# Optimization experiments

Measured on AMD Instinct MI355X. Metric: run time of the kernel, lower is better.

## Reference

```python
import jax, jax.numpy as jnp
import numpy as np

N, IN_C, HID, H1, E, EP = 4096, 256, 128, 4, 131072, 131072
TH, TL, FF = 4, 2, 512  # transformer heads, layers, ffn dim
D = HID  # transformer d_model


def setup_inputs() -> dict:
    key = jax.random.key(0)
    ks = jax.random.split(key, 32)
    s = 0.05
    inp = {
        'features': jax.random.normal(ks[0], (N, IN_C), jnp.float32),
        'src': jax.random.randint(ks[1], (E,), 0, N),
        'dst': jax.random.randint(ks[2], (E,), 0, N),
        'psrc': jax.random.randint(ks[3], (EP,), 0, N),
        'pdst': jax.random.randint(ks[4], (EP,), 0, N),
        # GAT layer 1: in=256 -> heads=4, out=128
        'W1': jax.random.normal(ks[5], (H1 * HID, IN_C), jnp.float32) * s,
        'al1': jax.random.normal(ks[6], (H1, HID), jnp.float32) * s,
        'ar1': jax.random.normal(ks[7], (H1, HID), jnp.float32) * s,
        'b1': jnp.zeros((H1 * HID,), jnp.float32),
        # GAT layer 2: in=512 -> heads=1, out=128
        'W2': jax.random.normal(ks[8], (HID, H1 * HID), jnp.float32) * s,
        'al2': jax.random.normal(ks[9], (1, HID), jnp.float32) * s,
        'ar2': jax.random.normal(ks[10], (1, HID), jnp.float32) * s,
        'b2': jnp.zeros((HID,), jnp.float32),
        # Transformer encoder (TL layers, torch TransformerEncoderLayer post-norm, relu)
        'tw_qkv': jax.random.normal(ks[11], (TL, 3 * D, D), jnp.float32) * s,
        'tb_qkv': jnp.zeros((TL, 3 * D), jnp.float32),
        'tw_o': jax.random.normal(ks[12], (TL, D, D), jnp.float32) * s,
        'tb_o': jnp.zeros((TL, D), jnp.float32),
        'ln1_g': jnp.ones((TL, D), jnp.float32),
        'ln1_b': jnp.zeros((TL, D), jnp.float32),
        'tw_ff1': jax.random.normal(ks[13], (TL, FF, D), jnp.float32) * s,
        'tb_ff1': jnp.zeros((TL, FF), jnp.float32),
        'tw_ff2': jax.random.normal(ks[14], (TL, D, FF), jnp.float32) * s,
        'tb_ff2': jnp.zeros((TL, D), jnp.float32),
        'ln2_g': jnp.ones((TL, D), jnp.float32),
        'ln2_b': jnp.zeros((TL, D), jnp.float32),
        # decoder MLP
        'fc1_w': jax.random.normal(ks[15], (HID, 2 * HID), jnp.float32) * s,
        'fc1_b': jnp.zeros((HID,), jnp.float32),
        'fc2_w': jax.random.normal(ks[16], (1, HID), jnp.float32) * s,
        'fc2_b': jnp.zeros((1,), jnp.float32),
    }
    return inp


def _leaky(x):
    return jnp.where(x > 0, x, 0.2 * x)


def _gat(x, W, al, ar, b, src, dst, n):
    H, F = al.shape
    h = (x @ W.T).reshape(n, H, F)  # [N,H,F]
    el = jnp.sum(h * al[None], -1)  # [N,H]
    er = jnp.sum(h * ar[None], -1)
    e = _leaky(el[src] + er[dst])  # [E,H]
    m = jax.ops.segment_max(e, dst, num_segments=n)
    ex = jnp.exp(e - m[dst])
    ssum = jax.ops.segment_sum(ex, dst, num_segments=n)
    alpha = ex / ssum[dst]  # edge softmax over incoming edges of dst
    out = jax.ops.segment_sum(h[src] * alpha[:, :, None], dst, num_segments=n)
    return out + b.reshape(1, H, F)


def _ln(x, g, b):
    mu = jnp.mean(x, -1, keepdims=True)
    var = jnp.mean((x - mu) ** 2, -1, keepdims=True)
    return (x - mu) / jnp.sqrt(var + 1e-5) * g + b


def _encoder_layer(h, wqkv, bqkv, wo, bo, g1, b1, wf1, bf1, wf2, bf2, g2, b2):
    n, d = h.shape
    hd = d // TH
    qkv = h @ wqkv.T + bqkv
    q, k, v = jnp.split(qkv, 3, axis=-1)
    q = q.reshape(n, TH, hd)
    k = k.reshape(n, TH, hd)
    v = v.reshape(n, TH, hd)
    scores = jnp.einsum('qhd,khd->hqk', q, k) / jnp.sqrt(jnp.float32(hd))
    attn = jax.nn.softmax(scores, axis=-1)
    o = jnp.einsum('hqk,khd->qhd', attn, v).reshape(n, d) @ wo.T + bo
    h = _ln(h + o, g1, b1)
    ff = jax.nn.relu(h @ wf1.T + bf1) @ wf2.T + bf2
    return _ln(h + ff, g2, b2)


def reference(features, W1, al1, ar1, b1, W2, al2, ar2, b2,
              tw_qkv, tb_qkv, tw_o, tb_o, ln1_g, ln1_b,
              tw_ff1, tb_ff1, tw_ff2, tb_ff2, ln2_g, ln2_b,
              fc1_w, fc1_b, fc2_w, fc2_b, src, dst, psrc, pdst):
    n = features.shape[0]
    h = _gat(features, W1, al1, ar1, b1, src, dst, n)  # [N,4,128]
    h = jax.nn.relu(h.reshape(n, -1))                  # [N,512]
    h = _gat(h, W2, al2, ar2, b2, src, dst, n)[:, 0]   # [N,128]
    for i in range(TL):
        h = _encoder_layer(h, tw_qkv[i], tb_qkv[i], tw_o[i], tb_o[i],
                           ln1_g[i], ln1_b[i], tw_ff1[i], tb_ff1[i],
                           tw_ff2[i], tb_ff2[i], ln2_g[i], ln2_b[i])
    ef = jnp.concatenate([h[psrc], h[pdst]], axis=1)   # [EP,256]
    x = jax.nn.relu(ef @ fc1_w.T + fc1_b)
    return jax.nn.sigmoid(x @ fc2_w.T + fc2_b)         # [EP,1]
```

## Files before the change

### kernel.cpp

```cpp
#include <hip/hip_runtime.h>
#include <hip/hip_bf16.h>
#include <math.h>

#define NN   4096
#define INC  256
#define HIDF 128
#define H1H  4
#define DM   128
#define THD  4
#define FFD  512

typedef __attribute__((ext_vector_type(8))) short bf16x8;
typedef __attribute__((ext_vector_type(4))) float f32x4;

__device__ __forceinline__ float leaky(float x){ return x > 0.f ? x : 0.2f*x; }

__device__ __forceinline__ ushort f2b(float f){
  __hip_bfloat16 h = __float2bfloat16(f);
  return __builtin_bit_cast(ushort, h);
}
__device__ __forceinline__ unsigned pk2(float a, float b){
  return (unsigned)f2b(a) | ((unsigned)f2b(b) << 16);
}
__device__ __forceinline__ float b2f(unsigned u){ return __uint_as_float(u << 16); }
__device__ __forceinline__ float b2flo(unsigned u){ return __uint_as_float(u << 16); }
__device__ __forceinline__ float b2fhi(unsigned u){ return __uint_as_float(u & 0xffff0000u); }

__device__ __forceinline__ int kvperm(int kv){
  return (kv & ~31) | ((kv & 12) << 1) | ((kv >> 2) & 4) | (kv & 3);
}

template<bool BIAS, bool RELU, bool OUTBF, bool ABF>
__global__ __launch_bounds__(256) void gemm_mf(
    const void* __restrict__ Av, const ushort* __restrict__ Wb,
    const float* __restrict__ bias, void* __restrict__ Cv,
    int M, int N, int K, int ldw)
{
  __shared__ uint4 As4[512];
  __shared__ uint4 Bs4[512];
  int tid = threadIdx.x;
  int row0 = blockIdx.y * 64, col0 = blockIdx.x * 64;
  int wid = tid >> 6, lane = tid & 63;
  int wm = wid >> 1, wn = wid & 1;
  int ql = lane & 15, g = lane >> 4;
  const f32x4 z4 = {0.f,0.f,0.f,0.f};
  f32x4 acc[2][2] = {z4,z4,z4,z4};

  for (int k0 = 0; k0 < K; k0 += 64) {
    #pragma unroll
    for (int p = 0; p < 2; p++) {
      int idx = tid + p*256;
      int ko = idx & 7, mm = idx >> 3;
      if constexpr (ABF) {
        As4[ko*64 + mm] = *(const uint4*)((const ushort*)Av + (size_t)(row0 + mm)*K + k0 + ko*8);
      } else {
        const float* sa = (const float*)Av + (size_t)(row0 + mm)*K + k0 + ko*8;
        float4 a0 = *(const float4*)sa;
        float4 a1 = *(const float4*)(sa + 4);
        uint4 av;
        av.x = pk2(a0.x, a0.y); av.y = pk2(a0.z, a0.w);
        av.z = pk2(a1.x, a1.y); av.w = pk2(a1.z, a1.w);
        As4[ko*64 + mm] = av;
      }
      Bs4[ko*64 + mm] = *(const uint4*)(Wb + (size_t)(col0 + mm)*ldw + k0 + ko*8);
    }
    __syncthreads();
    #pragma unroll
    for (int kk = 0; kk < 2; kk++) {
      int ko = kk*4 + g;
      bf16x8 a0 = *((const bf16x8*)As4 + ko*64 + wm*32 + ql);
      bf16x8 a1 = *((const bf16x8*)As4 + ko*64 + wm*32 + 16 + ql);
      bf16x8 b0 = *((const bf16x8*)Bs4 + ko*64 + wn*32 + ql);
      bf16x8 b1 = *((const bf16x8*)Bs4 + ko*64 + wn*32 + 16 + ql);
      acc[0][0] = __builtin_amdgcn_mfma_f32_16x16x32_bf16(a0, b0, acc[0][0], 0,0,0);
      acc[0][1] = __builtin_amdgcn_mfma_f32_16x16x32_bf16(a0, b1, acc[0][1], 0,0,0);
      acc[1][0] = __builtin_amdgcn_mfma_f32_16x16x32_bf16(a1, b0, acc[1][0], 0,0,0);
      acc[1][1] = __builtin_amdgcn_mfma_f32_16x16x32_bf16(a1, b1, acc[1][1], 0,0,0);
    }
    __syncthreads();
  }
  float bvs[2] = {0.f, 0.f};
  if (BIAS) {
    bvs[0] = bias[col0 + wn*32 + ql];
    bvs[1] = bias[col0 + wn*32 + 16 + ql];
  }
  #pragma unroll
  for (int fm = 0; fm < 2; fm++)
    #pragma unroll
    for (int fn = 0; fn < 2; fn++) {
      int row = row0 + wm*32 + fm*16 + g*4;
      int col = col0 + wn*32 + fn*16 + ql;
      #pragma unroll
      for (int r = 0; r < 4; r++) {
        float v = acc[fm][fn][r];
        if (BIAS) v += bvs[fn];
        if (RELU) v = fmaxf(v, 0.f);
        if (OUTBF) ((ushort*)Cv)[(size_t)(row + r)*N + col] = f2b(v);
        else       ((float*)Cv)[(size_t)(row + r)*N + col] = v;
      }
    }
}

__global__ __launch_bounds__(256) void gemm_qkv(
    const ushort* __restrict__ Ab, const ushort* __restrict__ Wb,
    const float* __restrict__ bias,
    ushort* __restrict__ qb, ushort* __restrict__ kt, ushort* __restrict__ vt)
{
  __shared__ uint4 As4[512];
  __shared__ uint4 Bs4[512];
  int tid = threadIdx.x;
  int row0 = blockIdx.y * 64, col0 = blockIdx.x * 64;
  int wid = tid >> 6, lane = tid & 63;
  int wm = wid >> 1, wn = wid & 1;
  int ql = lane & 15, g = lane >> 4;
  const f32x4 z4 = {0.f,0.f,0.f,0.f};
  f32x4 acc[2][2] = {z4,z4,z4,z4};

  for (int k0 = 0; k0 < 128; k0 += 64) {
    #pragma unroll
    for (int p = 0; p < 2; p++) {
      int idx = tid + p*256;
      int ko = idx & 7, mm = idx >> 3;
      As4[ko*64 + mm] = *(const uint4*)(Ab + (size_t)(row0 + mm)*128 + k0 + ko*8);
      Bs4[ko*64 + mm] = *(const uint4*)(Wb + (size_t)(col0 + mm)*128 + k0 + ko*8);
    }
    __syncthreads();
    #pragma unroll
    for (int kk = 0; kk < 2; kk++) {
      int ko = kk*4 + g;
      bf16x8 a0 = *((const bf16x8*)As4 + ko*64 + wm*32 + ql);
      bf16x8 a1 = *((const bf16x8*)As4 + ko*64 + wm*32 + 16 + ql);
      bf16x8 b0 = *((const bf16x8*)Bs4 + ko*64 + wn*32 + ql);
      bf16x8 b1 = *((const bf16x8*)Bs4 + ko*64 + wn*32 + 16 + ql);
      acc[0][0] = __builtin_amdgcn_mfma_f32_16x16x32_bf16(a0, b0, acc[0][0], 0,0,0);
      acc[0][1] = __builtin_amdgcn_mfma_f32_16x16x32_bf16(a0, b1, acc[0][1], 0,0,0);
      acc[1][0] = __builtin_amdgcn_mfma_f32_16x16x32_bf16(a1, b0, acc[1][0], 0,0,0);
      acc[1][1] = __builtin_amdgcn_mfma_f32_16x16x32_bf16(a1, b1, acc[1][1], 0,0,0);
    }
    __syncthreads();
  }
  float bvs[2];
  bvs[0] = bias[col0 + wn*32 + ql];
  bvs[1] = bias[col0 + wn*32 + 16 + ql];
  #pragma unroll
  for (int fm = 0; fm < 2; fm++)
    #pragma unroll
    for (int fn = 0; fn < 2; fn++) {
      int row = row0 + wm*32 + fm*16 + g*4;
      int col = col0 + wn*32 + fn*16 + ql;
      #pragma unroll
      for (int r = 0; r < 4; r++) {
        float v = acc[fm][fn][r] + bvs[fn];
        int kv = row + r;
        if (col < 128) {
          qb[(size_t)kv*128 + col] = f2b(v * 0.25505654708f);
        } else if (col < 256) {
          int hh = (col - 128) >> 5, d = (col - 128) & 31;
          kt[(size_t)hh*131072 + (size_t)kv*32 + d] = f2b(v);
        } else {
          int hh = (col - 256) >> 5, d = (col - 256) & 31;
          vt[(size_t)hh*131072 + (size_t)(kv >> 5)*1024 + (d >> 4)*512
             + (d & 15)*32 + kvperm(kv & 31)] = f2b(v);
        }
      }
    }
}

__global__ __launch_bounds__(256) void gemm_ln(
    const ushort* __restrict__ Ab, const ushort* __restrict__ Wb,
    const float* __restrict__ bias, ushort* __restrict__ h,
    const float* __restrict__ lng, const float* __restrict__ lnb, int K)
{
  __shared__ uint4 As4[512];
  __shared__ uint4 Bs4[1024];
  __shared__ float xs[64][132];
  int tid = threadIdx.x;
  int row0 = blockIdx.x * 64;
  int wid = tid >> 6, lane = tid & 63;
  int wm = wid >> 1, wn = wid & 1;
  int ql = lane & 15, g = lane >> 4;
  const f32x4 z4 = {0.f,0.f,0.f,0.f};
  f32x4 acc[2][4] = {z4,z4,z4,z4,z4,z4,z4,z4};

  for (int k0 = 0; k0 < K; k0 += 64) {
    #pragma unroll
    for (int p = 0; p < 2; p++) {
      int idx = tid + p*256;
      int ko = idx & 7, mm = idx >> 3;
      As4[ko*64 + mm] = *(const uint4*)(Ab + (size_t)(row0 + mm)*K + k0 + ko*8);
    }
    #pragma unroll
    for (int p = 0; p < 4; p++) {
      int idx = tid + p*256;
      int ko = idx & 7, nn = idx >> 3;
      Bs4[ko*128 + nn] = *(const uint4*)(Wb + (size_t)nn*K + k0 + ko*8);
    }
    __syncthreads();
    #pragma unroll
    for (int kk = 0; kk < 2; kk++) {
      int ko = kk*4 + g;
      bf16x8 a0 = *((const bf16x8*)As4 + ko*64 + wm*32 + ql);
      bf16x8 a1 = *((const bf16x8*)As4 + ko*64 + wm*32 + 16 + ql);
      #pragma unroll
      for (int fn = 0; fn < 4; fn++) {
        bf16x8 b = *((const bf16x8*)Bs4 + ko*128 + wn*64 + fn*16 + ql);
        acc[0][fn] = __builtin_amdgcn_mfma_f32_16x16x32_bf16(a0, b, acc[0][fn], 0,0,0);
        acc[1][fn] = __builtin_amdgcn_mfma_f32_16x16x32_bf16(a1, b, acc[1][fn], 0,0,0);
      }
    }
    __syncthreads();
  }
  #pragma unroll
  for (int fm = 0; fm < 2; fm++)
    #pragma unroll
    for (int fn = 0; fn < 4; fn++) {
      int rl = wm*32 + fm*16 + g*4;
      int col = wn*64 + fn*16 + ql;
      float bv = bias[col];
      #pragma unroll
      for (int r = 0; r < 4; r++) xs[rl + r][col] = acc[fm][fn][r] + bv;
    }
  __syncthreads();
  int rl = tid >> 2, c0 = (tid & 3) * 32;
  ushort* hrow = h + (size_t)(row0 + rl)*128;
  float s1 = 0.f, s2 = 0.f;
  #pragma unroll
  for (int i = 0; i < 8; i++) {
    uint2 rv = *(const uint2*)(hrow + c0 + i*4);
    float x0 = xs[rl][c0+i*4+0] + b2flo(rv.x);
    float x1 = xs[rl][c0+i*4+1] + b2fhi(rv.x);
    float x2 = xs[rl][c0+i*4+2] + b2flo(rv.y);
    float x3 = xs[rl][c0+i*4+3] + b2fhi(rv.y);
    xs[rl][c0+i*4+0] = x0; xs[rl][c0+i*4+1] = x1;
    xs[rl][c0+i*4+2] = x2; xs[rl][c0+i*4+3] = x3;
    s1 += x0 + x1 + x2 + x3;
    s2 += x0*x0 + x1*x1 + x2*x2 + x3*x3;
  }
  s1 += __shfl_xor(s1, 1); s1 += __shfl_xor(s1, 2);
  s2 += __shfl_xor(s2, 1); s2 += __shfl_xor(s2, 2);
  float mean = s1 * (1.f/128.f);
  float var  = s2 * (1.f/128.f) - mean*mean;
  float rstd = rsqrtf(var + 1e-5f);
  #pragma unroll
  for (int i = 0; i < 8; i++) {
    float4 g4 = *(const float4*)(lng + c0 + i*4);
    float4 b4 = *(const float4*)(lnb + c0 + i*4);
    float o0 = (xs[rl][c0+i*4+0] - mean)*rstd*g4.x + b4.x;
    float o1 = (xs[rl][c0+i*4+1] - mean)*rstd*g4.y + b4.y;
    float o2 = (xs[rl][c0+i*4+2] - mean)*rstd*g4.z + b4.z;
    float o3 = (xs[rl][c0+i*4+3] - mean)*rstd*g4.w + b4.w;
    uint2 ov; ov.x = pk2(o0, o1); ov.y = pk2(o2, o3);
    *(uint2*)(hrow + c0 + i*4) = ov;
  }
}

__global__ __launch_bounds__(256) void cvt_weights(
    const float* __restrict__ W1, const float* __restrict__ W2,
    const float* __restrict__ qkv, const float* __restrict__ o,
    const float* __restrict__ ff1, const float* __restrict__ ff2,
    const float* __restrict__ fc1, const float* __restrict__ fc1b,
    ushort* __restrict__ out, float* __restrict__ bias256)
{
  if (blockIdx.x == 608) {
    int t = threadIdx.x;
    bias256[t] = (t < 128) ? fc1b[t] : 0.f;
    return;
  }
  int i4 = (blockIdx.x*256 + threadIdx.x) * 4;
  const float* s; int loc;
  size_t dst = i4;
  if      (i4 < 131072) { s = W1;  loc = i4; }
  else if (i4 < 196608) { s = W2;  loc = i4 - 131072; }
  else if (i4 < 294912) { s = qkv; loc = i4 - 196608; }
  else if (i4 < 327680) { s = o;   loc = i4 - 294912; }
  else if (i4 < 458752) { s = ff1; loc = i4 - 327680; }
  else if (i4 < 589824) { s = ff2; loc = i4 - 458752; }
  else {
    s = fc1; loc = i4 - 589824;
    int j = loc >> 8, k2 = loc & 255;
    dst = 589824 + ((k2 >= 128) ? 16384 : 0) + j*128 + (k2 & 127);
  }
  float4 v = *(const float4*)(s + loc);
  uint2 w; w.x = pk2(v.x, v.y); w.y = pk2(v.z, v.w);
  *(uint2*)(out + dst) = w;
}

__global__ void zero_kernel(int* p, int n) {
  int i = blockIdx.x * blockDim.x + threadIdx.x;
  if (i < n) p[i] = 0;
}
__global__ void count_kernel(const int* __restrict__ dst, int* __restrict__ deg, int E) {
  int e = blockIdx.x * blockDim.x + threadIdx.x;
  if (e < E) atomicAdd(&deg[dst[e]], 1);
}
__global__ __launch_bounds__(1024) void scan_kernel(
    const int* __restrict__ deg, int* __restrict__ rowstart, int* __restrict__ cursor)
{
  __shared__ int sdata[1024];
  int t = threadIdx.x;
  int base = t * 4;
  int v0 = deg[base], v1 = deg[base+1], v2 = deg[base+2], v3 = deg[base+3];
  int tot = v0 + v1 + v2 + v3;
  sdata[t] = tot;
  __syncthreads();
  for (int off = 1; off < 1024; off <<= 1) {
    int x = (t >= off) ? sdata[t - off] : 0;
    __syncthreads();
    sdata[t] += x;
    __syncthreads();
  }
  int run = sdata[t] - tot;
  rowstart[base]   = run; cursor[base]   = run; run += v0;
  rowstart[base+1] = run; cursor[base+1] = run; run += v1;
  rowstart[base+2] = run; cursor[base+2] = run; run += v2;
  rowstart[base+3] = run; cursor[base+3] = run; run += v3;
  if (t == 1023) rowstart[4096] = run;
}
__global__ void fill_kernel(const int* __restrict__ src, const int* __restrict__ dst,
                            int* __restrict__ cursor, int* __restrict__ nbr, int E) {
  int e = blockIdx.x * blockDim.x + threadIdx.x;
  if (e < E) {
    int p = atomicAdd(&cursor[dst[e]], 1);
    nbr[p] = src[e];
  }
}

template<int H>
__global__ __launch_bounds__(256) void elr_kernel(
    const ushort* __restrict__ hmat, const float* __restrict__ al,
    const float* __restrict__ ar, float* __restrict__ el, float* __restrict__ er)
{
  int w = threadIdx.x >> 6, lane = threadIdx.x & 63;
  int n = blockIdx.x * 4 + w;
  if constexpr (H == 4) {
    int hh = lane >> 4, f0 = (lane & 15) * 8;
    bf16x8 hv = *(const bf16x8*)(hmat + (size_t)n*512 + hh*128 + f0);
    float4 a0 = *(const float4*)(al + hh*128 + f0);
    float4 a1 = *(const float4*)(al + hh*128 + f0 + 4);
    float4 r0 = *(const float4*)(ar + hh*128 + f0);
    float4 r1 = *(const float4*)(ar + hh*128 + f0 + 4);
    float x[8];
    #pragma unroll
    for (int i = 0; i < 8; i++) x[i] = b2f((ushort)hv[i]);
    float e1 = x[0]*a0.x + x[1]*a0.y + x[2]*a0.z + x[3]*a0.w
             + x[4]*a1.x + x[5]*a1.y + x[6]*a1.z + x[7]*a1.w;
    float e2 = x[0]*r0.x + x[1]*r0.y + x[2]*r0.z + x[3]*r0.w
             + x[4]*r1.x + x[5]*r1.y + x[6]*r1.z + x[7]*r1.w;
    #pragma unroll
    for (int s = 1; s < 16; s <<= 1) { e1 += __shfl_xor(e1, s); e2 += __shfl_xor(e2, s); }
    if ((lane & 15) == 0) { el[n*4 + hh] = e1; er[n*4 + hh] = e2; }
  } else {
    int f0 = lane * 2;
    unsigned u = *(const unsigned*)(hmat + (size_t)n*128 + f0);
    float x0 = b2flo(u), x1 = b2fhi(u);
    float2 av = *(const float2*)(al + f0);
    float2 rv = *(const float2*)(ar + f0);
    float e1 = x0*av.x + x1*av.y;
    float e2 = x0*rv.x + x1*rv.y;
    #pragma unroll
    for (int s = 1; s < 64; s <<= 1) { e1 += __shfl_xor(e1, s); e2 += __shfl_xor(e2, s); }
    if (lane == 0) { el[n] = e1; er[n] = e2; }
  }
}

__global__ __launch_bounds__(128) void gat_agg4(
    const ushort* __restrict__ hsrc, const float* __restrict__ el, const float* __restrict__ er,
    const int* __restrict__ rowstart, const int* __restrict__ nbr,
    const float* __restrict__ bias, ushort* __restrict__ out)
{
  int n = blockIdx.x, t = threadIdx.x;
  int e0 = rowstart[n];
  int deg = rowstart[n+1] - e0;
  __shared__ float red[128][4];
  __shared__ float mx_s[4], si_s[4];
  __shared__ float a_l[64][4];
  __shared__ int   s_l[64];
  float ernA[4];
  {
    float4 e4 = *(const float4*)(er + (size_t)n*4);
    ernA[0]=e4.x; ernA[1]=e4.y; ernA[2]=e4.z; ernA[3]=e4.w;
  }
  int hh = t >> 5, f0 = (t & 31) * 4;
  float ac0=0.f, ac1=0.f, ac2=0.f, ac3=0.f;
  if (deg > 0) {
    float mx[4] = {-INFINITY,-INFINITY,-INFINITY,-INFINITY};
    for (int i = t; i < deg; i += 128) {
      int s = nbr[e0 + i];
      float4 ev = *(const float4*)(el + (size_t)s*4);
      mx[0] = fmaxf(mx[0], leaky(ev.x + ernA[0]));
      mx[1] = fmaxf(mx[1], leaky(ev.y + ernA[1]));
      mx[2] = fmaxf(mx[2], leaky(ev.z + ernA[2]));
      mx[3] = fmaxf(mx[3], leaky(ev.w + ernA[3]));
    }
    #pragma unroll
    for (int h2 = 0; h2 < 4; h2++) red[t][h2] = mx[h2];
    __syncthreads();
    for (int st = 64; st > 0; st >>= 1) {
      if (t < st) {
        #pragma unroll
        for (int h2 = 0; h2 < 4; h2++) red[t][h2] = fmaxf(red[t][h2], red[t+st][h2]);
      }
      __syncthreads();
    }
    if (t < 4) mx_s[t] = red[0][t];
    __syncthreads();
    float se[4] = {};
    for (int i = t; i < deg; i += 128) {
      int s = nbr[e0 + i];
      float4 ev = *(const float4*)(el + (size_t)s*4);
      se[0] += __expf(leaky(ev.x + ernA[0]) - mx_s[0]);
      se[1] += __expf(leaky(ev.y + ernA[1]) - mx_s[1]);
      se[2] += __expf(leaky(ev.z + ernA[2]) - mx_s[2]);
      se[3] += __expf(leaky(ev.w + ernA[3]) - mx_s[3]);
    }
    #pragma unroll
    for (int h2 = 0; h2 < 4; h2++) red[t][h2] = se[h2];
    __syncthreads();
    for (int st = 64; st > 0; st >>= 1) {
      if (t < st) {
        #pragma unroll
        for (int h2 = 0; h2 < 4; h2++) red[t][h2] += red[t+st][h2];
      }
      __syncthreads();
    }
    if (t < 4) si_s[t] = 1.f / red[0][t];
    __syncthreads();
    for (int c = 0; c < deg; c += 64) {
      int cn = min(64, deg - c);
      if (t < cn) s_l[t] = nbr[e0 + c + t];
      for (int task = t; task < cn*4; task += 128) {
        int i = task >> 2, h2 = task & 3;
        int s = nbr[e0 + c + i];
        float v = leaky(el[(size_t)s*4 + h2] + ernA[h2]);
        a_l[i][h2] = __expf(v - mx_s[h2]) * si_s[h2];
      }
      __syncthreads();
      #pragma unroll 2
      for (int i = 0; i < cn; i++) {
        int s = s_l[i];
        float a = a_l[i][hh];
        uint2 hv = *(const uint2*)(hsrc + (size_t)s*512 + hh*128 + f0);
        ac0 += a * b2flo(hv.x);
        ac1 += a * b2fhi(hv.x);
        ac2 += a * b2flo(hv.y);
        ac3 += a * b2fhi(hv.y);
      }
      __syncthreads();
    }
  }
  const float* bp = bias + hh*128 + f0;
  float v0 = fmaxf(ac0 + bp[0], 0.f);
  float v1 = fmaxf(ac1 + bp[1], 0.f);
  float v2 = fmaxf(ac2 + bp[2], 0.f);
  float v3 = fmaxf(ac3 + bp[3], 0.f);
  uint2 ov; ov.x = pk2(v0, v1); ov.y = pk2(v2, v3);
  *(uint2*)(out + (size_t)n*512 + hh*128 + f0) = ov;
}

__global__ __launch_bounds__(128) void gat_agg1(
    const ushort* __restrict__ hsrc, const float* __restrict__ el, const float* __restrict__ er,
    const int* __restrict__ rowstart, const int* __restrict__ nbr,
    const float* __restrict__ bias, ushort* __restrict__ out)
{
  int n = blockIdx.x, t = threadIdx.x;
  int e0 = rowstart[n];
  int deg = rowstart[n+1] - e0;
  __shared__ float red[128];
  __shared__ float mx_s, si_s;
  __shared__ float a_l[64];
  __shared__ int   s_l[64];
  __shared__ float comb[2][64][2];
  float ern = er[n];
  int eo = t >> 6, f = (t & 63) * 2;
  float a0 = 0.f, a1 = 0.f;
  if (deg > 0) {
    float mx = -INFINITY;
    for (int i = t; i < deg; i += 128) {
      int s = nbr[e0 + i];
      mx = fmaxf(mx, leaky(el[s] + ern));
    }
    red[t] = mx; __syncthreads();
    for (int st = 64; st > 0; st >>= 1) {
      if (t < st) red[t] = fmaxf(red[t], red[t+st]);
      __syncthreads();
    }
    if (t == 0) mx_s = red[0];
    __syncthreads();
    float se = 0.f;
    for (int i = t; i < deg; i += 128) {
      int s = nbr[e0 + i];
      se += __expf(leaky(el[s] + ern) - mx_s);
    }
    red[t] = se; __syncthreads();
    for (int st = 64; st > 0; st >>= 1) {
      if (t < st) red[t] += red[t+st];
      __syncthreads();
    }
    if (t == 0) si_s = 1.f / red[0];
    __syncthreads();
    for (int c = 0; c < deg; c += 64) {
      int cn = min(64, deg - c);
      if (t < cn) {
        int s = nbr[e0 + c + t];
        s_l[t] = s;
        a_l[t] = __expf(leaky(el[s] + ern) - mx_s) * si_s;
      }
      __syncthreads();
      #pragma unroll 2
      for (int i = eo; i < cn; i += 2) {
        int s = s_l[i];
        float a = a_l[i];
        unsigned u = *(const unsigned*)(hsrc + (size_t)s*128 + f);
        a0 += a * b2flo(u);
        a1 += a * b2fhi(u);
      }
      __syncthreads();
    }
  }
  comb[eo][t & 63][0] = a0;
  comb[eo][t & 63][1] = a1;
  __syncthreads();
  if (t < 64) {
    float v0 = comb[0][t][0] + comb[1][t][0] + bias[t*2];
    float v1 = comb[0][t][1] + comb[1][t][1] + bias[t*2 + 1];
    *(unsigned*)(out + (size_t)n*128 + t*2) = pk2(v0, v1);
  }
}

#define LOADFRAGS(KF, VF, KV)                                              \
  {                                                                        \
    int _kv = (KV);                                                        \
    if (_kv < 1024) {                                                      \
      const ushort* _kp = kptr + (size_t)_kv * 32;                         \
      const ushort* _vp = vptr + (size_t)_kv * 32;                         \
      KF[0] = *(const bf16x8*)(_kp);                                       \
      KF[1] = *(const bf16x8*)(_kp + 512);                                 \
      KF[2] = *(const bf16x8*)(_kp + 1024);                                \
      KF[3] = *(const bf16x8*)(_kp + 1536);                                \
      VF[0] = *(const bf16x8*)(_vp);                                       \
      VF[1] = *(const bf16x8*)(_vp + 1024);                                \
      VF[2] = *(const bf16x8*)(_vp + 512);                                 \
      VF[3] = *(const bf16x8*)(_vp + 1536);                                \
    }                                                                      \
  }

#define QPASS(QF, LS, OA, OB, KF, VF)                                      \
  {                                                                        \
    f32x4 st0 = __builtin_amdgcn_mfma_f32_16x16x32_bf16(KF[0], QF, z4, 0, 0, 0); \
    f32x4 st1 = __builtin_amdgcn_mfma_f32_16x16x32_bf16(KF[1], QF, z4, 0, 0, 0); \
    f32x4 st2 = __builtin_amdgcn_mfma_f32_16x16x32_bf16(KF[2], QF, z4, 0, 0, 0); \
    f32x4 st3 = __builtin_amdgcn_mfma_f32_16x16x32_bf16(KF[3], QF, z4, 0, 0, 0); \
    float pvv[16];                                                         \
    _Pragma("unroll")                                                      \
    for (int i = 0; i < 4; i++) {                                          \
      pvv[i] = st0[i]; pvv[4+i] = st1[i]; pvv[8+i] = st2[i]; pvv[12+i] = st3[i]; \
    }                                                                      \
    _Pragma("unroll")                                                      \
    for (int i = 0; i < 16; i++) { pvv[i] = exp2f(pvv[i]); LS += pvv[i]; } \
    bf16x8 pf0 = { (short)f2b(pvv[0]),  (short)f2b(pvv[1]),  (short)f2b(pvv[2]),  (short)f2b(pvv[3]),   \
                   (short)f2b(pvv[4]),  (short)f2b(pvv[5]),  (short)f2b(pvv[6]),  (short)f2b(pvv[7]) }; \
    bf16x8 pf1 = { (short)f2b(pvv[8]),  (short)f2b(pvv[9]),  (short)f2b(pvv[10]), (short)f2b(pvv[11]),  \
                   (short)f2b(pvv[12]), (short)f2b(pvv[13]), (short)f2b(pvv[14]), (short)f2b(pvv[15]) };\
    OA = __builtin_amdgcn_mfma_f32_16x16x32_bf16(VF[0], pf0, OA, 0, 0, 0); \
    OA = __builtin_amdgcn_mfma_f32_16x16x32_bf16(VF[1], pf1, OA, 0, 0, 0); \
    OB = __builtin_amdgcn_mfma_f32_16x16x32_bf16(VF[2], pf0, OB, 0, 0, 0); \
    OB = __builtin_amdgcn_mfma_f32_16x16x32_bf16(VF[3], pf1, OB, 0, 0, 0); \
  }

#define ATTN_BODY(KF, VF, KN, VN, KV)                                      \
  {                                                                        \
    LOADFRAGS(KN, VN, (KV) + 64);                                          \
    QPASS(qf0, ls0, o00, o01, KF, VF);                                     \
    QPASS(qf1, ls1, o10, o11, KF, VF);                                     \
  }

__global__ __launch_bounds__(256) void attn_mfma(
    const ushort* __restrict__ qb,
    const ushort* __restrict__ kt,
    const ushort* __restrict__ vt,
    ushort* __restrict__ attnout)
{
  int lane = threadIdx.x & 63;
  int w    = threadIdx.x >> 6;
  int head = blockIdx.x >> 7;
  int q0   = (blockIdx.x & 127) * 32;
  int ql = lane & 15;
  int g  = lane >> 4;
  const f32x4 z4 = {0.f, 0.f, 0.f, 0.f};
  int kvbase = w * 1024;

  bf16x8 qf0 = *(const bf16x8*)(qb + (size_t)(q0 + ql)*128      + head*32 + g*8);
  bf16x8 qf1 = *(const bf16x8*)(qb + (size_t)(q0 + 16 + ql)*128 + head*32 + g*8);
  const ushort* kptr = kt + (size_t)head*131072 + (size_t)kvbase*32 + ql*32 + g*8;
  const ushort* vptr = vt + (size_t)head*131072 + (size_t)kvbase*32 + ql*32 + g*8;

  float ls0 = 0.f, ls1 = 0.f;
  f32x4 o00 = z4, o01 = z4, o10 = z4, o11 = z4;

  bf16x8 kfA[4], vfA[4], kfB[4], vfB[4];
  LOADFRAGS(kfA, vfA, 0);
  for (int kv0 = 0; kv0 < 1024; kv0 += 128) {
    ATTN_BODY(kfA, vfA, kfB, vfB, kv0);
    ATTN_BODY(kfB, vfB, kfA, vfA, kv0 + 64);
  }

  ls0 += __shfl_xor(ls0, 16); ls0 += __shfl_xor(ls0, 32);
  ls1 += __shfl_xor(ls1, 16); ls1 += __shfl_xor(ls1, 32);

  __shared__ float so[4][32][36];
  __shared__ float sl[4][32];
  if (g == 0) { sl[w][ql] = ls0; sl[w][16 + ql] = ls1; }
  #pragma unroll
  for (int r = 0; r < 4; r++) {
    so[w][ql][g*4 + r]           = o00[r];
    so[w][ql][16 + g*4 + r]      = o01[r];
    so[w][16 + ql][g*4 + r]      = o10[r];
    so[w][16 + ql][16 + g*4 + r] = o11[r];
  }
  __syncthreads();
  int q  = threadIdx.x >> 3;
  int d0 = (threadIdx.x & 7) * 4;
  float L = 0.f, O0 = 0.f, O1 = 0.f, O2 = 0.f, O3 = 0.f;
  #pragma unroll
  for (int w2 = 0; w2 < 4; w2++) {
    L  += sl[w2][q];
    O0 += so[w2][q][d0];
    O1 += so[w2][q][d0+1];
    O2 += so[w2][q][d0+2];
    O3 += so[w2][q][d0+3];
  }
  float rl = 1.f / L;
  uint2 w2v; w2v.x = pk2(O0*rl, O1*rl); w2v.y = pk2(O2*rl, O3*rl);
  *(uint2*)(attnout + (size_t)(q0 + q)*128 + head*32 + d0) = w2v;
}

__global__ __launch_bounds__(256) void pair_kernel(
    const ushort* __restrict__ ABp,
    const int* __restrict__ ps, const int* __restrict__ pd,
    const float* __restrict__ fc2w, const float* __restrict__ fc2b,
    float* __restrict__ out, int EP)
{
  int gw = (blockIdx.x * blockDim.x + threadIdx.x) >> 6;
  int lane = threadIdx.x & 63;
  int nw = (gridDim.x * blockDim.x) >> 6;
  float w0 = fc2w[2*lane], w1 = fc2w[2*lane + 1];
  float bb = fc2b[0];
  for (int p = gw; p < EP; p += nw) {
    int s = ps[p], d = pd[p];
    unsigned av = *(const unsigned*)(ABp + (size_t)s*256 + 2*lane);
    unsigned bv = *(const unsigned*)(ABp + (size_t)d*256 + 128 + 2*lane);
    float a0 = b2flo(av), a1 = b2fhi(av);
    float b0 = b2flo(bv), b1 = b2fhi(bv);
    float acc = fmaxf(a0 + b0, 0.f)*w0 + fmaxf(a1 + b1, 0.f)*w1;
    #pragma unroll
    for (int off = 32; off > 0; off >>= 1) acc += __shfl_down(acc, off);
    if (lane == 0) out[p] = 1.f / (1.f + __expf(-(acc + bb)));
  }
}

extern "C" void kernel_launch(void* const* d_in, const int* in_sizes, int n_in,
                              void* d_out, int out_size, void* d_ws, size_t ws_size,
                              hipStream_t stream)
{
  const float* features = (const float*)d_in[0];
  const int*   src      = (const int*)d_in[1];
  const int*   dst      = (const int*)d_in[2];
  const int*   psrc     = (const int*)d_in[3];
  const int*   pdst     = (const int*)d_in[4];
  const float* W1   = (const float*)d_in[5];
  const float* al1  = (const float*)d_in[6];
  const float* ar1  = (const float*)d_in[7];
  const float* b1   = (const float*)d_in[8];
  const float* W2   = (const float*)d_in[9];
  const float* al2  = (const float*)d_in[10];
  const float* ar2  = (const float*)d_in[11];
  const float* b2   = (const float*)d_in[12];
  const float* tw_qkv = (const float*)d_in[13];
  const float* tb_qkv = (const float*)d_in[14];
  const float* tw_o   = (const float*)d_in[15];
  const float* tb_o   = (const float*)d_in[16];
  const float* ln1_g  = (const float*)d_in[17];
  const float* ln1_b  = (const float*)d_in[18];
  const float* tw_ff1 = (const float*)d_in[19];
  const float* tb_ff1 = (const float*)d_in[20];
  const float* tw_ff2 = (const float*)d_in[21];
  const float* tb_ff2 = (const float*)d_in[22];
  const float* ln2_g  = (const float*)d_in[23];
  const float* ln2_b  = (const float*)d_in[24];
  const float* fc1_w  = (const float*)d_in[25];
  const float* fc1_b  = (const float*)d_in[26];
  const float* fc2_w  = (const float*)d_in[27];
  const float* fc2_b  = (const float*)d_in[28];
  int E  = in_sizes[1];
  int EP = in_sizes[3];

  float* ws = (float*)d_ws;
  size_t off = 0;
  auto alloc = [&](size_t n) { float* p = ws + off; off += n; return p; };
  ushort* hb    = (ushort*)alloc((size_t)NN * 64);
  ushort* h1b   = (ushort*)alloc((size_t)NN * 256);
  ushort* h2b   = (ushort*)alloc((size_t)NN * 256);
  ushort* bigb  = (ushort*)alloc((size_t)NN * 256);
  ushort* hgb   = (ushort*)alloc((size_t)NN * 64);
  ushort* qb    = (ushort*)alloc((size_t)NN * 64);
  ushort* attnb = (ushort*)alloc((size_t)NN * 64);
  ushort* kt    = (ushort*)alloc((size_t)NN * 64);
  ushort* vt    = (ushort*)alloc((size_t)NN * 64);
  ushort* wbf   = (ushort*)alloc(622592/2);
  ushort* ABp   = (ushort*)alloc((size_t)NN * 128);
  float*  bias256 = alloc(256);
  float*  el1   = alloc((size_t)NN * 4);
  float*  er1   = alloc((size_t)NN * 4);
  float*  el2   = alloc((size_t)NN);
  float*  er2   = alloc((size_t)NN);
  int* ibase    = (int*)(ws + off);
  int* deg      = ibase;
  int* rowstart = ibase + 4096;
  int* cursor   = ibase + 4096 + 4097;
  int* nbr      = cursor + 4096;

  const size_t oW1 = 0, oW2 = 131072, oQKV = 196608, oO = 294912,
               oFF1 = 327680, oFF2 = 458752, oFC1 = 589824;

  cvt_weights<<<609, 256, 0, stream>>>(W1, W2, tw_qkv, tw_o, tw_ff1, tw_ff2,
                                       fc1_w, fc1_b, wbf, bias256);

  zero_kernel<<<16, 256, 0, stream>>>(deg, 4096);
  count_kernel<<<(E + 255)/256, 256, 0, stream>>>(dst, deg, E);
  scan_kernel<<<1, 1024, 0, stream>>>(deg, rowstart, cursor);
  fill_kernel<<<(E + 255)/256, 256, 0, stream>>>(src, dst, cursor, nbr, E);

  gemm_mf<false,false,true,false><<<dim3(8, 64), 256, 0, stream>>>(
      features, wbf + oW1, nullptr, h1b, NN, 512, 256, 256);
  elr_kernel<4><<<1024, 256, 0, stream>>>(h1b, al1, ar1, el1, er1);
  gat_agg4<<<NN, 128, 0, stream>>>(h1b, el1, er1, rowstart, nbr, b1, h2b);

  gemm_mf<false,false,true,true><<<dim3(2, 64), 256, 0, stream>>>(
      h2b, wbf + oW2, nullptr, hgb, NN, 128, 512, 512);
  elr_kernel<1><<<1024, 256, 0, stream>>>(hgb, al2, ar2, el2, er2);
  gat_agg1<<<NN, 128, 0, stream>>>(hgb, el2, er2, rowstart, nbr, b2, hb);

  for (int l = 0; l < 2; l++) {
    gemm_qkv<<<dim3(6, 64), 256, 0, stream>>>(
        hb, wbf + oQKV + (size_t)l*49152, tb_qkv + l*384, qb, kt, vt);
    attn_mfma<<<512, 256, 0, stream>>>(qb, kt, vt, attnb);
    gemm_ln<<<64, 256, 0, stream>>>(
        attnb, wbf + oO + (size_t)l*16384, tb_o + l*128, hb,
        ln1_g + l*128, ln1_b + l*128, 128);
    gemm_mf<true,true,true,true><<<dim3(8, 64), 256, 0, stream>>>(
        hb, wbf + oFF1 + (size_t)l*65536, tb_ff1 + l*512, bigb, NN, 512, 128, 128);
    gemm_ln<<<64, 256, 0, stream>>>(
        bigb, wbf + oFF2 + (size_t)l*65536, tb_ff2 + l*128, hb,
        ln2_g + l*128, ln2_b + l*128, 512);
  }

  gemm_mf<true,false,true,true><<<dim3(4, 64), 256, 0, stream>>>(
      hb, wbf + oFC1, bias256, ABp, NN, 256, 128, 128);
  pair_kernel<<<1024, 256, 0, stream>>>(ABp, psrc, pdst, fc2_w, fc2_b, (float*)d_out, EP);
}
```

Before: 240.3 us.

## Retile gemm_ln to 16 rows, warp-per-node GAT aggregation, fused CSR build

gemm_ln now processes 16 rows per block instead of 64, so it launches 256 blocks instead of 64 and fills more compute units. Both GAT aggregation kernels are rewritten to assign one wavefront per destination node. Their reductions use shuffles instead of shared-memory trees with block barriers, and attention weights are staged in 256-edge chunks. The zero, count and scan kernels are merged into one single-block kernel that counts degrees with shared-memory atomics, which removes launches but serialises the counting of all edges on one block.

```diff
diff --git a/kernel.cpp b/kernel.cpp
--- a/kernel.cpp
+++ b/kernel.cpp
@@ -171,23 +171,20 @@
     const float* __restrict__ bias, ushort* __restrict__ h,
     const float* __restrict__ lng, const float* __restrict__ lnb, int K)
 {
-  __shared__ uint4 As4[512];
+  __shared__ uint4 As4[128];
   __shared__ uint4 Bs4[1024];
-  __shared__ float xs[64][132];
+  __shared__ float xs[16][132];
   int tid = threadIdx.x;
-  int row0 = blockIdx.x * 64;
-  int wid = tid >> 6, lane = tid & 63;
-  int wm = wid >> 1, wn = wid & 1;
+  int row0 = blockIdx.x * 16;
+  int wv = tid >> 6, lane = tid & 63;
   int ql = lane & 15, g = lane >> 4;
   const f32x4 z4 = {0.f,0.f,0.f,0.f};
-  f32x4 acc[2][4] = {z4,z4,z4,z4,z4,z4,z4,z4};
+  f32x4 acc[2] = {z4, z4};
 
   for (int k0 = 0; k0 < K; k0 += 64) {
-    #pragma unroll
-    for (int p = 0; p < 2; p++) {
-      int idx = tid + p*256;
-      int ko = idx & 7, mm = idx >> 3;
-      As4[ko*64 + mm] = *(const uint4*)(Ab + (size_t)(row0 + mm)*K + k0 + ko*8);
+    if (tid < 128) {
+      int ko = tid & 7, mm = tid >> 3;
+      As4[ko*16 + mm] = *(const uint4*)(Ab + (size_t)(row0 + mm)*K + k0 + ko*8);
     }
     #pragma unroll
     for (int p = 0; p < 4; p++) {
@@ -199,59 +196,54 @@
     #pragma unroll
     for (int kk = 0; kk < 2; kk++) {
       int ko = kk*4 + g;
-      bf16x8 a0 = *((const bf16x8*)As4 + ko*64 + wm*32 + ql);
-      bf16x8 a1 = *((const bf16x8*)As4 + ko*64 + wm*32 + 16 + ql);
+      bf16x8 a = *((const bf16x8*)As4 + ko*16 + ql);
       #pragma unroll
-      for (int fn = 0; fn < 4; fn++) {
-        bf16x8 b = *((const bf16x8*)Bs4 + ko*128 + wn*64 + fn*16 + ql);
-        acc[0][fn] = __builtin_amdgcn_mfma_f32_16x16x32_bf16(a0, b, acc[0][fn], 0,0,0);
-        acc[1][fn] = __builtin_amdgcn_mfma_f32_16x16x32_bf16(a1, b, acc[1][fn], 0,0,0);
+      for (int fn = 0; fn < 2; fn++) {
+        bf16x8 b = *((const bf16x8*)Bs4 + ko*128 + wv*32 + fn*16 + ql);
+        acc[fn] = __builtin_amdgcn_mfma_f32_16x16x32_bf16(a, b, acc[fn], 0,0,0);
       }
     }
     __syncthreads();
   }
   #pragma unroll
-  for (int fm = 0; fm < 2; fm++)
-    #pragma unroll
-    for (int fn = 0; fn < 4; fn++) {
-      int rl = wm*32 + fm*16 + g*4;
-      int col = wn*64 + fn*16 + ql;
-      float bv = bias[col];
-      #pragma unroll
-      for (int r = 0; r < 4; r++) xs[rl + r][col] = acc[fm][fn][r] + bv;
-    }
+  for (int fn = 0; fn < 2; fn++) {
+    int col = wv*32 + fn*16 + ql;
+    float bv = bias[col];
+    #pragma unroll
+    for (int r = 0; r < 4; r++) xs[g*4 + r][col] = acc[fn][r] + bv;
+  }
   __syncthreads();
-  int rl = tid >> 2, c0 = (tid & 3) * 32;
+  int rl = tid >> 4, cl = tid & 15, c0 = cl * 8;
   ushort* hrow = h + (size_t)(row0 + rl)*128;
+  uint4 rv = *(const uint4*)(hrow + c0);
+  float x[8];
+  x[0] = xs[rl][c0+0] + b2flo(rv.x); x[1] = xs[rl][c0+1] + b2fhi(rv.x);
+  x[2] = xs[rl][c0+2] + b2flo(rv.y); x[3] = xs[rl][c0+3] + b2fhi(rv.y);
+  x[4] = xs[rl][c0+4] + b2flo(rv.z); x[5] = xs[rl][c0+5] + b2fhi(rv.z);
+  x[6] = xs[rl][c0+6] + b2flo(rv.w); x[7] = xs[rl][c0+7] + b2fhi(rv.w);
   float s1 = 0.f, s2 = 0.f;
   #pragma unroll
-  for (int i = 0; i < 8; i++) {
-    uint2 rv = *(const uint2*)(hrow + c0 + i*4);
-    float x0 = xs[rl][c0+i*4+0] + b2flo(rv.x);
-    float x1 = xs[rl][c0+i*4+1] + b2fhi(rv.x);
-    float x2 = xs[rl][c0+i*4+2] + b2flo(rv.y);
-    float x3 = xs[rl][c0+i*4+3] + b2fhi(rv.y);
-    xs[rl][c0+i*4+0] = x0; xs[rl][c0+i*4+1] = x1;
-    xs[rl][c0+i*4+2] = x2; xs[rl][c0+i*4+3] = x3;
-    s1 += x0 + x1 + x2 + x3;
-    s2 += x0*x0 + x1*x1 + x2*x2 + x3*x3;
-  }
-  s1 += __shfl_xor(s1, 1); s1 += __shfl_xor(s1, 2);
-  s2 += __shfl_xor(s2, 1); s2 += __shfl_xor(s2, 2);
+  for (int i = 0; i < 8; i++) { s1 += x[i]; s2 += x[i]*x[i]; }
+  #pragma unroll
+  for (int st = 1; st < 16; st <<= 1) {
+    s1 += __shfl_xor(s1, st); s2 += __shfl_xor(s2, st);
+  }
   float mean = s1 * (1.f/128.f);
   float var  = s2 * (1.f/128.f) - mean*mean;
   float rstd = rsqrtf(var + 1e-5f);
-  #pragma unroll
-  for (int i = 0; i < 8; i++) {
-    float4 g4 = *(const float4*)(lng + c0 + i*4);
-    float4 b4 = *(const float4*)(lnb + c0 + i*4);
-    float o0 = (xs[rl][c0+i*4+0] - mean)*rstd*g4.x + b4.x;
-    float o1 = (xs[rl][c0+i*4+1] - mean)*rstd*g4.y + b4.y;
-    float o2 = (xs[rl][c0+i*4+2] - mean)*rstd*g4.z + b4.z;
-    float o3 = (xs[rl][c0+i*4+3] - mean)*rstd*g4.w + b4.w;
-    uint2 ov; ov.x = pk2(o0, o1); ov.y = pk2(o2, o3);
-    *(uint2*)(hrow + c0 + i*4) = ov;
-  }
+  float o[8];
+  #pragma unroll
+  for (int i = 0; i < 8; i += 4) {
+    float4 g4 = *(const float4*)(lng + c0 + i);
+    float4 b4 = *(const float4*)(lnb + c0 + i);
+    o[i+0] = (x[i+0]-mean)*rstd*g4.x + b4.x;
+    o[i+1] = (x[i+1]-mean)*rstd*g4.y + b4.y;
+    o[i+2] = (x[i+2]-mean)*rstd*g4.z + b4.z;
+    o[i+3] = (x[i+3]-mean)*rstd*g4.w + b4.w;
+  }
+  uint4 ov; ov.x = pk2(o[0],o[1]); ov.y = pk2(o[2],o[3]);
+  ov.z = pk2(o[4],o[5]); ov.w = pk2(o[6],o[7]);
+  *(uint4*)(hrow + c0) = ov;
 }
 
 __global__ __launch_bounds__(256) void cvt_weights(
@@ -285,31 +277,30 @@
   *(uint2*)(out + dst) = w;
 }
 
-__global__ void zero_kernel(int* p, int n) {
-  int i = blockIdx.x * blockDim.x + threadIdx.x;
-  if (i < n) p[i] = 0;
-}
-__global__ void count_kernel(const int* __restrict__ dst, int* __restrict__ deg, int E) {
-  int e = blockIdx.x * blockDim.x + threadIdx.x;
-  if (e < E) atomicAdd(&deg[dst[e]], 1);
-}
-__global__ __launch_bounds__(1024) void scan_kernel(
-    const int* __restrict__ deg, int* __restrict__ rowstart, int* __restrict__ cursor)
-{
-  __shared__ int sdata[1024];
+__global__ __launch_bounds__(1024) void csr_build(
+    const int* __restrict__ dst, int* __restrict__ rowstart,
+    int* __restrict__ cursor, int E)
+{
+  __shared__ int sdeg[4096];
+  __shared__ int ssum[1024];
   int t = threadIdx.x;
+  #pragma unroll
+  for (int i = 0; i < 4; i++) sdeg[t + i*1024] = 0;
+  __syncthreads();
+  for (int e = t; e < E; e += 1024) atomicAdd(&sdeg[dst[e]], 1);
+  __syncthreads();
   int base = t * 4;
-  int v0 = deg[base], v1 = deg[base+1], v2 = deg[base+2], v3 = deg[base+3];
+  int v0 = sdeg[base], v1 = sdeg[base+1], v2 = sdeg[base+2], v3 = sdeg[base+3];
   int tot = v0 + v1 + v2 + v3;
-  sdata[t] = tot;
+  ssum[t] = tot;
   __syncthreads();
   for (int off = 1; off < 1024; off <<= 1) {
-    int x = (t >= off) ? sdata[t - off] : 0;
+    int x = (t >= off) ? ssum[t - off] : 0;
     __syncthreads();
-    sdata[t] += x;
+    ssum[t] += x;
     __syncthreads();
   }
-  int run = sdata[t] - tot;
+  int run = ssum[t] - tot;
   rowstart[base]   = run; cursor[base]   = run; run += v0;
   rowstart[base+1] = run; cursor[base+1] = run; run += v1;
   rowstart[base+2] = run; cursor[base+2] = run; run += v2;
@@ -363,168 +354,128 @@
   }
 }
 
-__global__ __launch_bounds__(128) void gat_agg4(
+__global__ __launch_bounds__(256) void gat_agg4(
     const ushort* __restrict__ hsrc, const float* __restrict__ el, const float* __restrict__ er,
     const int* __restrict__ rowstart, const int* __restrict__ nbr,
     const float* __restrict__ bias, ushort* __restrict__ out)
 {
-  int n = blockIdx.x, t = threadIdx.x;
+  __shared__ float s_alpha[4][256][4];
+  __shared__ int   s_nbr[4][256];
+  int wv = threadIdx.x >> 6, lane = threadIdx.x & 63;
+  int n = blockIdx.x * 4 + wv;
   int e0 = rowstart[n];
   int deg = rowstart[n+1] - e0;
-  __shared__ float red[128][4];
-  __shared__ float mx_s[4], si_s[4];
-  __shared__ float a_l[64][4];
-  __shared__ int   s_l[64];
-  float ernA[4];
-  {
-    float4 e4 = *(const float4*)(er + (size_t)n*4);
-    ernA[0]=e4.x; ernA[1]=e4.y; ernA[2]=e4.z; ernA[3]=e4.w;
-  }
-  int hh = t >> 5, f0 = (t & 31) * 4;
-  float ac0=0.f, ac1=0.f, ac2=0.f, ac3=0.f;
+  float4 ern = *(const float4*)(er + (size_t)n*4);
+  int hh = lane >> 4;
+  float acc[8] = {};
   if (deg > 0) {
-    float mx[4] = {-INFINITY,-INFINITY,-INFINITY,-INFINITY};
-    for (int i = t; i < deg; i += 128) {
+    float m0=-1e30f, m1=-1e30f, m2=-1e30f, m3=-1e30f;
+    for (int i = lane; i < deg; i += 64) {
       int s = nbr[e0 + i];
       float4 ev = *(const float4*)(el + (size_t)s*4);
-      mx[0] = fmaxf(mx[0], leaky(ev.x + ernA[0]));
-      mx[1] = fmaxf(mx[1], leaky(ev.y + ernA[1]));
-      mx[2] = fmaxf(mx[2], leaky(ev.z + ernA[2]));
-      mx[3] = fmaxf(mx[3], leaky(ev.w + ernA[3]));
-    }
-    #pragma unroll
-    for (int h2 = 0; h2 < 4; h2++) red[t][h2] = mx[h2];
-    __syncthreads();
-    for (int st = 64; st > 0; st >>= 1) {
-      if (t < st) {
-        #pragma unroll
-        for (int h2 = 0; h2 < 4; h2++) red[t][h2] = fmaxf(red[t][h2], red[t+st][h2]);
-      }
-      __syncthreads();
-    }
-    if (t < 4) mx_s[t] = red[0][t];
-    __syncthreads();
-    float se[4] = {};
-    for (int i = t; i < deg; i += 128) {
+      m0 = fmaxf(m0, leaky(ev.x + ern.x));
+      m1 = fmaxf(m1, leaky(ev.y + ern.y));
+      m2 = fmaxf(m2, leaky(ev.z + ern.z));
+      m3 = fmaxf(m3, leaky(ev.w + ern.w));
+    }
+    #pragma unroll
+    for (int st = 1; st < 64; st <<= 1) {
+      m0 = fmaxf(m0, __shfl_xor(m0, st)); m1 = fmaxf(m1, __shfl_xor(m1, st));
+      m2 = fmaxf(m2, __shfl_xor(m2, st)); m3 = fmaxf(m3, __shfl_xor(m3, st));
+    }
+    float se0=0.f, se1=0.f, se2=0.f, se3=0.f;
+    for (int i = lane; i < deg; i += 64) {
       int s = nbr[e0 + i];
       float4 ev = *(const float4*)(el + (size_t)s*4);
-      se[0] += __expf(leaky(ev.x + ernA[0]) - mx_s[0]);
-      se[1] += __expf(leaky(ev.y + ernA[1]) - mx_s[1]);
-      se[2] += __expf(leaky(ev.z + ernA[2]) - mx_s[2]);
-      se[3] += __expf(leaky(ev.w + ernA[3]) - mx_s[3]);
-    }
-    #pragma unroll
-    for (int h2 = 0; h2 < 4; h2++) red[t][h2] = se[h2];
-    __syncthreads();
-    for (int st = 64; st > 0; st >>= 1) {
-      if (t < st) {
-        #pragma unroll
-        for (int h2 = 0; h2 < 4; h2++) red[t][h2] += red[t+st][h2];
+      se0 += __expf(leaky(ev.x + ern.x) - m0);
+      se1 += __expf(leaky(ev.y + ern.y) - m1);
+      se2 += __expf(leaky(ev.z + ern.z) - m2);
+      se3 += __expf(leaky(ev.w + ern.w) - m3);
+    }
+    #pragma unroll
+    for (int st = 1; st < 64; st <<= 1) {
+      se0 += __shfl_xor(se0, st); se1 += __shfl_xor(se1, st);
+      se2 += __shfl_xor(se2, st); se3 += __shfl_xor(se3, st);
+    }
+    float si0 = 1.f/se0, si1 = 1.f/se1, si2 = 1.f/se2, si3 = 1.f/se3;
+    for (int c = 0; c < deg; c += 256) {
+      int cn = min(256, deg - c);
+      for (int i = lane; i < cn; i += 64) {
+        int s = nbr[e0 + c + i];
+        s_nbr[wv][i] = s;
+        float4 ev = *(const float4*)(el + (size_t)s*4);
+        s_alpha[wv][i][0] = __expf(leaky(ev.x + ern.x) - m0) * si0;
+        s_alpha[wv][i][1] = __expf(leaky(ev.y + ern.y) - m1) * si1;
+        s_alpha[wv][i][2] = __expf(leaky(ev.z + ern.z) - m2) * si2;
+        s_alpha[wv][i][3] = __expf(leaky(ev.w + ern.w) - m3) * si3;
       }
-      __syncthreads();
-    }
-    if (t < 4) si_s[t] = 1.f / red[0][t];
-    __syncthreads();
-    for (int c = 0; c < deg; c += 64) {
-      int cn = min(64, deg - c);
-      if (t < cn) s_l[t] = nbr[e0 + c + t];
-      for (int task = t; task < cn*4; task += 128) {
-        int i = task >> 2, h2 = task & 3;
-        int s = nbr[e0 + c + i];
-        float v = leaky(el[(size_t)s*4 + h2] + ernA[h2]);
-        a_l[i][h2] = __expf(v - mx_s[h2]) * si_s[h2];
+      #pragma unroll 4
+      for (int i = 0; i < cn; i++) {
+        float a = s_alpha[wv][i][hh];
+        int s = s_nbr[wv][i];
+        uint4 hv = *(const uint4*)(hsrc + (size_t)s*512 + lane*8);
+        acc[0] += a * b2flo(hv.x); acc[1] += a * b2fhi(hv.x);
+        acc[2] += a * b2flo(hv.y); acc[3] += a * b2fhi(hv.y);
+        acc[4] += a * b2flo(hv.z); acc[5] += a * b2fhi(hv.z);
+        acc[6] += a * b2flo(hv.w); acc[7] += a * b2fhi(hv.w);
       }
-      __syncthreads();
-      #pragma unroll 2
-      for (int i = 0; i < cn; i++) {
-        int s = s_l[i];
-        float a = a_l[i][hh];
-        uint2 hv = *(const uint2*)(hsrc + (size_t)s*512 + hh*128 + f0);
-        ac0 += a * b2flo(hv.x);
-        ac1 += a * b2fhi(hv.x);
-        ac2 += a * b2flo(hv.y);
-        ac3 += a * b2fhi(hv.y);
-      }
-      __syncthreads();
-    }
-  }
-  const float* bp = bias + hh*128 + f0;
-  float v0 = fmaxf(ac0 + bp[0], 0.f);
-  float v1 = fmaxf(ac1 + bp[1], 0.f);
-  float v2 = fmaxf(ac2 + bp[2], 0.f);
-  float v3 = fmaxf(ac3 + bp[3], 0.f);
-  uint2 ov; ov.x = pk2(v0, v1); ov.y = pk2(v2, v3);
-  *(uint2*)(out + (size_t)n*512 + hh*128 + f0) = ov;
-}
-
-__global__ __launch_bounds__(128) void gat_agg1(
+    }
+  }
+  const float* bp = bias + lane*8;
+  float4 b0 = *(const float4*)(bp);
+  float4 b1 = *(const float4*)(bp + 4);
+  float v0 = fmaxf(acc[0]+b0.x, 0.f), v1 = fmaxf(acc[1]+b0.y, 0.f);
+  float v2 = fmaxf(acc[2]+b0.z, 0.f), v3 = fmaxf(acc[3]+b0.w, 0.f);
+  float v4 = fmaxf(acc[4]+b1.x, 0.f), v5 = fmaxf(acc[5]+b1.y, 0.f);
+  float v6 = fmaxf(acc[6]+b1.z, 0.f), v7 = fmaxf(acc[7]+b1.w, 0.f);
+  uint4 ov; ov.x = pk2(v0,v1); ov.y = pk2(v2,v3); ov.z = pk2(v4,v5); ov.w = pk2(v6,v7);
+  *(uint4*)(out + (size_t)n*512 + lane*8) = ov;
+}
+
+__global__ __launch_bounds__(256) void gat_agg1(
     const ushort* __restrict__ hsrc, const float* __restrict__ el, const float* __restrict__ er,
     const int* __restrict__ rowstart, const int* __restrict__ nbr,
     const float* __restrict__ bias, ushort* __restrict__ out)
 {
-  int n = blockIdx.x, t = threadIdx.x;
+  __shared__ float s_alpha[4][256];
+  __shared__ int   s_nbr[4][256];
+  int wv = threadIdx.x >> 6, lane = threadIdx.x & 63;
+  int n = blockIdx.x * 4 + wv;
   int e0 = rowstart[n];
   int deg = rowstart[n+1] - e0;
-  __shared__ float red[128];
-  __shared__ float mx_s, si_s;
-  __shared__ float a_l[64];
-  __shared__ int   s_l[64];
-  __shared__ float comb[2][64][2];
   float ern = er[n];
-  int eo = t >> 6, f = (t & 63) * 2;
   float a0 = 0.f, a1 = 0.f;
   if (deg > 0) {
-    float mx = -INFINITY;
-    for (int i = t; i < deg; i += 128) {
-      int s = nbr[e0 + i];
-      mx = fmaxf(mx, leaky(el[s] + ern));
-    }
-    red[t] = mx; __syncthreads();
-    for (int st = 64; st > 0; st >>= 1) {
-      if (t < st) red[t] = fmaxf(red[t], red[t+st]);
-      __syncthreads();
-    }
-    if (t == 0) mx_s = red[0];
-    __syncthreads();
+    float mx = -1e30f;
+    for (int i = lane; i < deg; i += 64)
+      mx = fmaxf(mx, leaky(el[nbr[e0 + i]] + ern));
+    #pragma unroll
+    for (int st = 1; st < 64; st <<= 1) mx = fmaxf(mx, __shfl_xor(mx, st));
     float se = 0.f;
-    for (int i = t; i < deg; i += 128) {
-      int s = nbr[e0 + i];
-      se += __expf(leaky(el[s] + ern) - mx_s);
-    }
-    red[t] = se; __syncthreads();
-    for (int st = 64; st > 0; st >>= 1) {
-      if (t < st) red[t] += red[t+st];
-      __syncthreads();
-    }
-    if (t == 0) si_s = 1.f / red[0];
-    __syncthreads();
-    for (int c = 0; c < deg; c += 64) {
-      int cn = min(64, deg - c);
-      if (t < cn) {
-        int s = nbr[e0 + c + t];
-        s_l[t] = s;
-        a_l[t] = __expf(leaky(el[s] + ern) - mx_s) * si_s;
+    for (int i = lane; i < deg; i += 64)
+      se += __expf(leaky(el[nbr[e0 + i]] + ern) - mx);
+    #pragma unroll
+    for (int st = 1; st < 64; st <<= 1) se += __shfl_xor(se, st);
+    float si = 1.f / se;
+    for (int c = 0; c < deg; c += 256) {
+      int cn = min(256, deg - c);
+      for (int i = lane; i < cn; i += 64) {
+        int s = nbr[e0 + c + i];
+        s_nbr[wv][i] = s;
+        s_alpha[wv][i] = __expf(leaky(el[s] + ern) - mx) * si;
       }
-      __syncthreads();
-      #pragma unroll 2
-      for (int i = eo; i < cn; i += 2) {
-        int s = s_l[i];
-        float a = a_l[i];
-        unsigned u = *(const unsigned*)(hsrc + (size_t)s*128 + f);
+      #pragma unroll 4
+      for (int i = 0; i < cn; i++) {
+        float a = s_alpha[wv][i];
+        int s = s_nbr[wv][i];
+        unsigned u = *(const unsigned*)(hsrc + (size_t)s*128 + lane*2);
         a0 += a * b2flo(u);
         a1 += a * b2fhi(u);
       }
-      __syncthreads();
-    }
-  }
-  comb[eo][t & 63][0] = a0;
-  comb[eo][t & 63][1] = a1;
-  __syncthreads();
-  if (t < 64) {
-    float v0 = comb[0][t][0] + comb[1][t][0] + bias[t*2];
-    float v1 = comb[0][t][1] + comb[1][t][1] + bias[t*2 + 1];
-    *(unsigned*)(out + (size_t)n*128 + t*2) = pk2(v0, v1);
-  }
+    }
+  }
+  float v0 = a0 + bias[lane*2], v1 = a1 + bias[lane*2 + 1];
+  *(unsigned*)(out + (size_t)n*128 + lane*2) = pk2(v0, v1);
 }
 
 #define LOADFRAGS(KF, VF, KV)                                              \
@@ -714,9 +665,8 @@
   float*  el2   = alloc((size_t)NN);
   float*  er2   = alloc((size_t)NN);
   int* ibase    = (int*)(ws + off);
-  int* deg      = ibase;
-  int* rowstart = ibase + 4096;
-  int* cursor   = ibase + 4096 + 4097;
+  int* rowstart = ibase;
+  int* cursor   = ibase + 4097;
   int* nbr      = cursor + 4096;
 
   const size_t oW1 = 0, oW2 = 131072, oQKV = 196608, oO = 294912,
@@ -725,31 +675,29 @@
   cvt_weights<<<609, 256, 0, stream>>>(W1, W2, tw_qkv, tw_o, tw_ff1, tw_ff2,
                                        fc1_w, fc1_b, wbf, bias256);
 
-  zero_kernel<<<16, 256, 0, stream>>>(deg, 4096);
-  count_kernel<<<(E + 255)/256, 256, 0, stream>>>(dst, deg, E);
-  scan_kernel<<<1, 1024, 0, stream>>>(deg, rowstart, cursor);
+  csr_build<<<1, 1024, 0, stream>>>(dst, rowstart, cursor, E);
   fill_kernel<<<(E + 255)/256, 256, 0, stream>>>(src, dst, cursor, nbr, E);
 
   gemm_mf<false,false,true,false><<<dim3(8, 64), 256, 0, stream>>>(
       features, wbf + oW1, nullptr, h1b, NN, 512, 256, 256);
   elr_kernel<4><<<1024, 256, 0, stream>>>(h1b, al1, ar1, el1, er1);
-  gat_agg4<<<NN, 128, 0, stream>>>(h1b, el1, er1, rowstart, nbr, b1, h2b);
+  gat_agg4<<<1024, 256, 0, stream>>>(h1b, el1, er1, rowstart, nbr, b1, h2b);
 
   gemm_mf<false,false,true,true><<<dim3(2, 64), 256, 0, stream>>>(
       h2b, wbf + oW2, nullptr, hgb, NN, 128, 512, 512);
   elr_kernel<1><<<1024, 256, 0, stream>>>(hgb, al2, ar2, el2, er2);
-  gat_agg1<<<NN, 128, 0, stream>>>(hgb, el2, er2, rowstart, nbr, b2, hb);
+  gat_agg1<<<1024, 256, 0, stream>>>(hgb, el2, er2, rowstart, nbr, b2, hb);
 
   for (int l = 0; l < 2; l++) {
     gemm_qkv<<<dim3(6, 64), 256, 0, stream>>>(
         hb, wbf + oQKV + (size_t)l*49152, tb_qkv + l*384, qb, kt, vt);
     attn_mfma<<<512, 256, 0, stream>>>(qb, kt, vt, attnb);
-    gemm_ln<<<64, 256, 0, stream>>>(
+    gemm_ln<<<256, 256, 0, stream>>>(
         attnb, wbf + oO + (size_t)l*16384, tb_o + l*128, hb,
         ln1_g + l*128, ln1_b + l*128, 128);
     gemm_mf<true,true,true,true><<<dim3(8, 64), 256, 0, stream>>>(
         hb, wbf + oFF1 + (size_t)l*65536, tb_ff1 + l*512, bigb, NN, 512, 128, 128);
-    gemm_ln<<<64, 256, 0, stream>>>(
+    gemm_ln<<<256, 256, 0, stream>>>(
         bigb, wbf + oFF2 + (size_t)l*65536, tb_ff2 + l*128, hb,
         ln2_g + l*128, ln2_b + l*128, 512);
   }
```

Result: no change. 242.2 us (+0.8%).
